# Optimization experiments

Measured on AMD Instinct MI355X. Metric: run time of the kernel, lower is better.

## Reference

```python
import jax, jax.numpy as jnp
import numpy as np

B, S, D, H = 4, 2048, 1024, 16
HD = D // H


def setup_inputs() -> dict:
    key = jax.random.key(0)
    ks = jax.random.split(key, 9)
    s = 1.0 / np.sqrt(D)
    return {
        "x": jax.random.normal(ks[0], (B, S, D), dtype=jnp.float32),
        "Wq": jax.random.uniform(ks[1], (D, D), jnp.float32, -s, s),
        "bq": jax.random.uniform(ks[2], (D,), jnp.float32, -s, s),
        "Wk": jax.random.uniform(ks[3], (D, D), jnp.float32, -s, s),
        "bk": jax.random.uniform(ks[4], (D,), jnp.float32, -s, s),
        "Wv": jax.random.uniform(ks[5], (D, D), jnp.float32, -s, s),
        "bv": jax.random.uniform(ks[6], (D,), jnp.float32, -s, s),
        "Wo": jax.random.uniform(ks[7], (D, D), jnp.float32, -s, s),
        "bo": jax.random.uniform(ks[8], (D,), jnp.float32, -s, s),
    }


def reference(x, Wq, bq, Wk, bk, Wv, bv, Wo, bo):
    b, s, _ = x.shape
    # projections (torch Linear: y = x @ W.T + b; here W stored as [D,D], use x@W for equivalent math)
    q = (x @ Wq + bq).reshape(b, s, H, HD).transpose(0, 2, 1, 3)  # [b,h,s,hd]
    k = (x @ Wk + bk).reshape(b, s, H, HD).transpose(0, 2, 1, 3)
    v = (x @ Wv + bv).reshape(b, s, H, HD).transpose(0, 2, 1, 3)
    scale = 1.0 / np.sqrt(HD).astype(np.float32)
    scores = jnp.einsum("bhqd,bhkd->bhqk", q, k) * scale  # [b,h,s,s]
    attn = jax.nn.softmax(scores, axis=-1)
    out = jnp.einsum("bhqk,bhkd->bhqd", attn, v)  # [b,h,s,hd]
    out = out.transpose(0, 2, 1, 3).reshape(b, s, D)
    return out @ Wo + bo
```

## Files before the change

kernel.cpp:

```cpp
#include <hip/hip_runtime.h>
#include <hip/hip_bf16.h>

#define NB 4
#define NS 2048
#define ND 1024
#define NH 16
#define NHD 64
#define NM (NB * NS)

typedef __attribute__((ext_vector_type(8))) short bf16x8;
typedef __attribute__((ext_vector_type(4))) float f32x4;
typedef __attribute__((ext_vector_type(16))) float f32x16;
typedef __attribute__((ext_vector_type(4))) unsigned int u32x4;

typedef const unsigned int __attribute__((address_space(1)))* gas_t;
typedef unsigned int __attribute__((address_space(3)))* las_t;

__device__ __forceinline__ void gload_lds16(const void* g, void* l) {
  __builtin_amdgcn_global_load_lds((gas_t)g, (las_t)l, 16, 0, 0);
}

__device__ __forceinline__ unsigned short f2bf(float f) {
  union { __hip_bfloat16 h; unsigned short u; } cv;
  cv.h = __float2bfloat16(f);
  return cv.u;
}

__device__ __forceinline__ unsigned int cvtpk(float a, float b) {
  unsigned int r;
  asm("v_cvt_pk_bf16_f32 %0, %1, %2" : "=v"(r) : "v"(a), "v"(b));
  return r;
}

__device__ __forceinline__ float fexp2(float x) {
  return __builtin_amdgcn_exp2f(x);
}

__global__ __launch_bounds__(256) void convert_x(
    const float* __restrict__ in, uint4* __restrict__ out) {
  const int c = blockIdx.x * 256 + threadIdx.x;
  const float4 a = *(const float4*)(in + (size_t)c * 8);
  const float4 b = *(const float4*)(in + (size_t)c * 8 + 4);
  uint4 u;
  u.x = cvtpk(a.x, a.y); u.y = cvtpk(a.z, a.w);
  u.z = cvtpk(b.x, b.y); u.w = cvtpk(b.z, b.w);
  out[c] = u;
}

__global__ __launch_bounds__(256) void transpose_qkv(
    const float* __restrict__ Wq, const float* __restrict__ Wk,
    const float* __restrict__ Wv, unsigned short* __restrict__ out) {
  __shared__ float tile[64][65];
  const int t = threadIdx.x;
  const int bx = blockIdx.x;
  const int by = blockIdx.y;
  const int which = by >> 4;
  const float* in = which == 0 ? Wq : (which == 1 ? Wk : Wv);
  const int byl = by & 15;
#pragma unroll
  for (int j = 0; j < 4; ++j) {
    const int lin = j * 1024 + t * 4;
    const int r = lin >> 6, c = lin & 63;
    float4 v = *(const float4*)(in + (size_t)(bx * 64 + r) * ND + byl * 64 + c);
    tile[r][c + 0] = v.x; tile[r][c + 1] = v.y;
    tile[r][c + 2] = v.z; tile[r][c + 3] = v.w;
  }
  __syncthreads();
#pragma unroll
  for (int j = 0; j < 4; ++j) {
    const int lin = j * 1024 + t * 4;
    const int r = lin >> 6, c = lin & 63;
    uint2 u;
    u.x = cvtpk(tile[c + 0][r], tile[c + 1][r]);
    u.y = cvtpk(tile[c + 2][r], tile[c + 3][r]);
    *(uint2*)(out + (size_t)(by * 64 + r) * ND + bx * 64 + c) = u;
  }
}

__global__ __launch_bounds__(256) void transpose_w(
    const float* __restrict__ in, unsigned short* __restrict__ out) {
  __shared__ float tile[64][65];
  const int t = threadIdx.x;
  const int bx = blockIdx.x, by = blockIdx.y;
#pragma unroll
  for (int j = 0; j < 4; ++j) {
    const int lin = j * 1024 + t * 4;
    const int r = lin >> 6, c = lin & 63;
    float4 v = *(const float4*)(in + (size_t)(bx * 64 + r) * ND + by * 64 + c);
    tile[r][c + 0] = v.x; tile[r][c + 1] = v.y;
    tile[r][c + 2] = v.z; tile[r][c + 3] = v.w;
  }
  __syncthreads();
#pragma unroll
  for (int j = 0; j < 4; ++j) {
    const int lin = j * 1024 + t * 4;
    const int r = lin >> 6, c = lin & 63;
    uint2 u;
    u.x = cvtpk(tile[c + 0][r], tile[c + 1][r]);
    u.y = cvtpk(tile[c + 2][r], tile[c + 3][r]);
    *(uint2*)(out + (size_t)(by * 64 + r) * ND + bx * 64 + c) = u;
  }
}

__global__ __launch_bounds__(256) void gemm_qkv(
    const unsigned short* __restrict__ Ab, const unsigned short* __restrict__ BT,
    const float* __restrict__ bq, const float* __restrict__ bk,
    const float* __restrict__ bv, unsigned short* __restrict__ Qb,
    unsigned short* __restrict__ Kb, unsigned short* __restrict__ VTb) {
  __shared__ unsigned short As[128 * 32];
  __shared__ unsigned short Bs[128 * 32];
  const int t = threadIdx.x;
  const int w = blockIdx.x;
  const int xcd = w & 7, idx = w >> 3;
  const int mblk = xcd + ((idx / 24) << 3);
  const int nblk = idx % 24;
  const int m0 = mblk * 128, n0 = nblk * 128;
  const int lane = t & 63, wid = t >> 6;
  const int wm = (wid >> 1) * 64, wn = (wid & 1) * 64;
  const int lr = lane & 15, lg = lane >> 4;

  const f32x4 zero4 = {0.f, 0.f, 0.f, 0.f};
  f32x4 acc[4][4];
#pragma unroll
  for (int i = 0; i < 4; ++i)
#pragma unroll
    for (int j = 0; j < 4; ++j) acc[i][j] = zero4;

  for (int k0 = 0; k0 < ND; k0 += 32) {
    __syncthreads();
#pragma unroll
    for (int j = 0; j < 2; ++j) {
      const int idx2 = j * 256 + t;
      const int row = idx2 >> 2, cs = idx2 & 3;
      const int cg = cs ^ ((row >> 1) & 3);
      gload_lds16(BT + (size_t)(n0 + row) * ND + k0 + cg * 8, &Bs[idx2 * 8]);
      gload_lds16(Ab + (size_t)(m0 + row) * ND + k0 + cg * 8, &As[idx2 * 8]);
    }
    __syncthreads();

    bf16x8 af[4], bv4[4];
#pragma unroll
    for (int mi = 0; mi < 4; ++mi) {
      const int row = wm + mi * 16 + lr;
      const int slot = lg ^ ((row >> 1) & 3);
      af[mi] = *(const bf16x8*)&As[row * 32 + slot * 8];
    }
#pragma unroll
    for (int ni = 0; ni < 4; ++ni) {
      const int row = wn + ni * 16 + lr;
      const int slot = lg ^ ((row >> 1) & 3);
      bv4[ni] = *(const bf16x8*)&Bs[row * 32 + slot * 8];
    }
    __builtin_amdgcn_s_setprio(1);
#pragma unroll
    for (int mi = 0; mi < 4; ++mi)
#pragma unroll
      for (int ni = 0; ni < 4; ++ni)
        acc[mi][ni] = __builtin_amdgcn_mfma_f32_16x16x32_bf16(
            af[mi], bv4[ni], acc[mi][ni], 0, 0, 0);
    __builtin_amdgcn_s_setprio(0);
  }

#pragma unroll
  for (int mi = 0; mi < 4; ++mi) {
#pragma unroll
    for (int ni = 0; ni < 4; ++ni) {
      const int mbase = m0 + wm + mi * 16 + lg * 4;
      const int n = n0 + wn + ni * 16 + lr;
      const int which = n >> 10, nl = n & 1023;
      const int h = nl >> 6, hd = nl & 63;
      const float bval = which == 0 ? bq[nl] : (which == 1 ? bk[nl] : bv[nl]);
      float vo[4];
#pragma unroll
      for (int i = 0; i < 4; ++i) {
        vo[i] = acc[mi][ni][i] + bval;
        if (which == 0) vo[i] *= 0.18033688f;
      }
      if (which < 2) {
        unsigned short* dst = which == 0 ? Qb : Kb;
#pragma unroll
        for (int i = 0; i < 4; ++i) {
          const int m = mbase + i;
          const int b = m >> 11, s = m & (NS - 1);
          dst[(((size_t)b * NH + h) * NS + s) * NHD + hd] = f2bf(vo[i]);
        }
      } else {
        const int b = mbase >> 11, s = mbase & (NS - 1);
        ushort4 o;
        o.x = f2bf(vo[0]); o.y = f2bf(vo[1]);
        o.z = f2bf(vo[2]); o.w = f2bf(vo[3]);
        *(ushort4*)&VTb[(((size_t)b * NH + h) * NHD + hd) * NS + s] = o;
      }
    }
  }
}

__global__ __launch_bounds__(256) void gemm_out(
    const unsigned short* __restrict__ Ab, const unsigned short* __restrict__ BT,
    const float* __restrict__ bias, float* __restrict__ Cf) {
  __shared__ unsigned short As[128 * 32];
  __shared__ unsigned short Bs[128 * 32];
  const int t = threadIdx.x;
  const int w = blockIdx.x;
  const int mblk = (w & 7) + ((w >> 6) << 3);
  const int nblk = (w >> 3) & 7;
  const int m0 = mblk * 128, n0 = nblk * 128;
  const int lane = t & 63, wid = t >> 6;
  const int wm = (wid >> 1) * 64, wn = (wid & 1) * 64;
  const int lr = lane & 15, lg = lane >> 4;

  const f32x4 zero4 = {0.f, 0.f, 0.f, 0.f};
  f32x4 acc[4][4];
#pragma unroll
  for (int i = 0; i < 4; ++i)
#pragma unroll
    for (int j = 0; j < 4; ++j) acc[i][j] = zero4;

  for (int k0 = 0; k0 < ND; k0 += 32) {
    __syncthreads();
#pragma unroll
    for (int j = 0; j < 2; ++j) {
      const int idx2 = j * 256 + t;
      const int row = idx2 >> 2, cs = idx2 & 3;
      const int cg = cs ^ ((row >> 1) & 3);
      gload_lds16(BT + (size_t)(n0 + row) * ND + k0 + cg * 8, &Bs[idx2 * 8]);
      gload_lds16(Ab + (size_t)(m0 + row) * ND + k0 + cg * 8, &As[idx2 * 8]);
    }
    __syncthreads();

    bf16x8 af[4], bv4[4];
#pragma unroll
    for (int mi = 0; mi < 4; ++mi) {
      const int row = wm + mi * 16 + lr;
      const int slot = lg ^ ((row >> 1) & 3);
      af[mi] = *(const bf16x8*)&As[row * 32 + slot * 8];
    }
#pragma unroll
    for (int ni = 0; ni < 4; ++ni) {
      const int row = wn + ni * 16 + lr;
      const int slot = lg ^ ((row >> 1) & 3);
      bv4[ni] = *(const bf16x8*)&Bs[row * 32 + slot * 8];
    }
    __builtin_amdgcn_s_setprio(1);
#pragma unroll
    for (int mi = 0; mi < 4; ++mi)
#pragma unroll
      for (int ni = 0; ni < 4; ++ni)
        acc[mi][ni] = __builtin_amdgcn_mfma_f32_16x16x32_bf16(
            af[mi], bv4[ni], acc[mi][ni], 0, 0, 0);
    __builtin_amdgcn_s_setprio(0);
  }

#pragma unroll
  for (int mi = 0; mi < 4; ++mi) {
#pragma unroll
    for (int ni = 0; ni < 4; ++ni) {
      const int mbase = m0 + wm + mi * 16 + lg * 4;
      const int n = n0 + wn + ni * 16 + lr;
      const float bval = bias[n];
#pragma unroll
      for (int i = 0; i < 4; ++i)
        Cf[(size_t)(mbase + i) * ND + n] = acc[mi][ni][i] + bval;
    }
  }
}

__global__ __launch_bounds__(512) void attn_mfma(
    const unsigned short* __restrict__ Qb, const unsigned short* __restrict__ Kb,
    const unsigned short* __restrict__ VTb, unsigned short* __restrict__ Aout) {
  __shared__ unsigned short S[32768];
  const int t = threadIdx.x, lane = t & 63, wid = t >> 6;
  const int lq = lane & 31, h = lane >> 5;
  const int w = blockIdx.x;
  const int xcd = w & 7, idx = w >> 3;
  const int bh = xcd + ((idx >> 3) << 3);
  const int qtile = idx & 7;
  const size_t hoff = (size_t)bh * NS * NHD;
  const int q0w = qtile * 256 + wid * 32;

  bf16x8 qf[4];
#pragma unroll
  for (int kc = 0; kc < 4; ++kc)
    qf[kc] = *(const bf16x8*)(Qb + hoff + (size_t)(q0w + lq) * NHD + kc * 16 + h * 8);

  const unsigned short* gK[2];
  const unsigned short* gV[2];
  unsigned short* lK[2];
  unsigned short* lV[2];
#pragma unroll
  for (int j = 0; j < 2; ++j) {
    const int c16 = wid * 2 + j;
    gK[j] = Kb + hoff + (size_t)((c16 & 3) * 32 + lq) * NHD + (c16 >> 2) * 16 + h * 8;
    lK[j] = &S[c16 * 512];
    gV[j] = VTb + hoff + (size_t)((c16 & 1) * 32 + lq) * NS + (c16 >> 1) * 16 + h * 8;
    lV[j] = &S[16384 + c16 * 512];
  }

  f32x16 z16 = 0.f;
  f32x16 oacc0 = 0.f, oacc1 = 0.f, lacc = 0.f;
  const short oneb = (short)0x3F80;
  const bf16x8 ones = {oneb, oneb, oneb, oneb, oneb, oneb, oneb, oneb};

  auto stage = [&](int bufofs, int tl) {
    const int kt = (2 * qtile + tl) & 15;
    const size_t kOff = (size_t)kt * (128 * NHD);
    const size_t vOff = (size_t)kt * 128;
#pragma unroll
    for (int j = 0; j < 2; ++j) {
      gload_lds16(gK[j] + kOff, lK[j] + bufofs);
      gload_lds16(gV[j] + vOff, lV[j] + bufofs);
    }
  };

  auto compute = [&](int bufofs) {
    const unsigned short* kb = &S[bufofs] + lane * 8;
    const unsigned short* vb = &S[16384 + bufofs] + lane * 8;
#pragma unroll
    for (int sb = 0; sb < 4; ++sb) {
      __builtin_amdgcn_s_setprio(1);
      f32x16 s;
      {
        bf16x8 k0 = *(const bf16x8*)(kb + sb * 512);
        s = __builtin_amdgcn_mfma_f32_32x32x16_bf16(k0, qf[0], z16, 0, 0, 0);
        bf16x8 k1 = *(const bf16x8*)(kb + sb * 512 + 2048);
        s = __builtin_amdgcn_mfma_f32_32x32x16_bf16(k1, qf[1], s, 0, 0, 0);
        bf16x8 k2 = *(const bf16x8*)(kb + sb * 512 + 4096);
        s = __builtin_amdgcn_mfma_f32_32x32x16_bf16(k2, qf[2], s, 0, 0, 0);
        bf16x8 k3 = *(const bf16x8*)(kb + sb * 512 + 6144);
        s = __builtin_amdgcn_mfma_f32_32x32x16_bf16(k3, qf[3], s, 0, 0, 0);
      }
      __builtin_amdgcn_s_setprio(0);

      unsigned int a0, a1, b0, b1, c0, c1, d0, d1;
      a0 = cvtpk(fexp2(s[0]), fexp2(s[1]));
      a1 = cvtpk(fexp2(s[2]), fexp2(s[3]));
      b0 = cvtpk(fexp2(s[4]), fexp2(s[5]));
      b1 = cvtpk(fexp2(s[6]), fexp2(s[7]));
      c0 = cvtpk(fexp2(s[8]), fexp2(s[9]));
      c1 = cvtpk(fexp2(s[10]), fexp2(s[11]));
      d0 = cvtpk(fexp2(s[12]), fexp2(s[13]));
      d1 = cvtpk(fexp2(s[14]), fexp2(s[15]));
      asm("v_permlane32_swap_b32 %0, %1" : "+v"(a0), "+v"(b0));
      asm("v_permlane32_swap_b32 %0, %1" : "+v"(a1), "+v"(b1));
      asm("v_permlane32_swap_b32 %0, %1" : "+v"(c0), "+v"(d0));
      asm("v_permlane32_swap_b32 %0, %1" : "+v"(c1), "+v"(d1));
      u32x4 plo_u = {a0, a1, b0, b1};
      u32x4 phi_u = {c0, c1, d0, d1};
      const bf16x8 plo = __builtin_bit_cast(bf16x8, plo_u);
      const bf16x8 phi = __builtin_bit_cast(bf16x8, phi_u);

      const int cA = sb * 2048;
      __builtin_amdgcn_s_setprio(1);
      {
        bf16x8 v0 = *(const bf16x8*)(vb + cA);
        oacc0 = __builtin_amdgcn_mfma_f32_32x32x16_bf16(v0, plo, oacc0, 0, 0, 0);
        bf16x8 v1 = *(const bf16x8*)(vb + cA + 512);
        oacc1 = __builtin_amdgcn_mfma_f32_32x32x16_bf16(v1, plo, oacc1, 0, 0, 0);
        lacc = __builtin_amdgcn_mfma_f32_32x32x16_bf16(ones, plo, lacc, 0, 0, 0);
        bf16x8 v2 = *(const bf16x8*)(vb + cA + 1024);
        oacc0 = __builtin_amdgcn_mfma_f32_32x32x16_bf16(v2, phi, oacc0, 0, 0, 0);
        bf16x8 v3 = *(const bf16x8*)(vb + cA + 1536);
        oacc1 = __builtin_amdgcn_mfma_f32_32x32x16_bf16(v3, phi, oacc1, 0, 0, 0);
        lacc = __builtin_amdgcn_mfma_f32_32x32x16_bf16(ones, phi, lacc, 0, 0, 0);
      }
      __builtin_amdgcn_s_setprio(0);
    }
  };

  stage(0, 0);
  __syncthreads();

  for (int i = 0; i < 8; ++i) {
    stage(8192, 2 * i + 1);
    compute(0);
    __syncthreads();
    if (i < 7) stage(0, 2 * i + 2);
    compute(8192);
    __syncthreads();
  }

  const float inv = 1.0f / lacc[0];
  unsigned short* Olds = &S[wid * 2304];
#pragma unroll
  for (int rr = 0; rr < 8; ++rr) {
    const int dl = 2 * (rr & 1) + 8 * (rr >> 1) + 4 * h;
    *(unsigned int*)&Olds[lq * 72 + dl] =
        cvtpk(oacc0[2 * rr] * inv, oacc0[2 * rr + 1] * inv);
    *(unsigned int*)&Olds[lq * 72 + 32 + dl] =
        cvtpk(oacc1[2 * rr] * inv, oacc1[2 * rr + 1] * inv);
  }
  const int b = bh >> 4, hh = bh & 15;
#pragma unroll
  for (int jj = 0; jj < 4; ++jj) {
    const int ci = jj * 64 + lane;
    const int q = ci >> 3, slot = ci & 7;
    const uint4 ov = *(const uint4*)&Olds[q * 72 + slot * 8];
    const int m = b * NS + q0w + q;
    *(uint4*)&Aout[(size_t)m * ND + hh * NHD + slot * 8] = ov;
  }
}

extern "C" void kernel_launch(void* const* d_in, const int* in_sizes, int n_in,
                              void* d_out, int out_size, void* d_ws,
                              size_t ws_size, hipStream_t stream) {
  const float* x  = (const float*)d_in[0];
  const float* Wq = (const float*)d_in[1];
  const float* bq = (const float*)d_in[2];
  const float* Wk = (const float*)d_in[3];
  const float* bk = (const float*)d_in[4];
  const float* Wv = (const float*)d_in[5];
  const float* bv = (const float*)d_in[6];
  const float* Wo = (const float*)d_in[7];
  const float* bo = (const float*)d_in[8];
  float* out = (float*)d_out;

  const size_t BIG = (size_t)NM * ND;
  unsigned short* Qb    = (unsigned short*)d_ws;
  unsigned short* Kb    = Qb + BIG;
  unsigned short* VTb   = Kb + BIG;
  unsigned short* Aattn = VTb + BIG;
  unsigned short* WTqkv = Aattn;
  unsigned short* WTo   = Qb;
  unsigned short* xb    = (unsigned short*)d_out;

  convert_x<<<4096, 256, 0, stream>>>(x, (uint4*)xb);
  transpose_qkv<<<dim3(16, 48), 256, 0, stream>>>(Wq, Wk, Wv, WTqkv);
  gemm_qkv<<<1536, 256, 0, stream>>>(xb, WTqkv, bq, bk, bv, Qb, Kb, VTb);

  attn_mfma<<<512, 512, 0, stream>>>(Qb, Kb, VTb, Aattn);

  transpose_w<<<dim3(16, 16), 256, 0, stream>>>(Wo, WTo);
  gemm_out<<<512, 256, 0, stream>>>(Aattn, WTo, bo, out);
}
```

Measured before the change: 190.2 us.

## Double-buffer LDS tiles in projection GEMMs and remap QKV block order

```diff
diff --git a/kernel.cpp b/kernel.cpp
--- a/kernel.cpp
+++ b/kernel.cpp
@@ -107,13 +107,13 @@
     const float* __restrict__ bq, const float* __restrict__ bk,
     const float* __restrict__ bv, unsigned short* __restrict__ Qb,
     unsigned short* __restrict__ Kb, unsigned short* __restrict__ VTb) {
-  __shared__ unsigned short As[128 * 32];
-  __shared__ unsigned short Bs[128 * 32];
+  __shared__ unsigned short As[2][128 * 32];
+  __shared__ unsigned short Bs[2][128 * 32];
   const int t = threadIdx.x;
   const int w = blockIdx.x;
   const int xcd = w & 7, idx = w >> 3;
-  const int mblk = xcd + ((idx / 24) << 3);
-  const int nblk = idx % 24;
+  const int nblk = xcd * 3 + idx % 3;
+  const int mblk = idx / 3;
   const int m0 = mblk * 128, n0 = nblk * 128;
   const int lane = t & 63, wid = t >> 6;
   const int wm = (wid >> 1) * 64, wn = (wid & 1) * 64;
@@ -126,30 +126,30 @@
 #pragma unroll
     for (int j = 0; j < 4; ++j) acc[i][j] = zero4;
 
-  for (int k0 = 0; k0 < ND; k0 += 32) {
-    __syncthreads();
+  auto stage = [&](int k0, int buf) {
 #pragma unroll
     for (int j = 0; j < 2; ++j) {
       const int idx2 = j * 256 + t;
       const int row = idx2 >> 2, cs = idx2 & 3;
       const int cg = cs ^ ((row >> 1) & 3);
-      gload_lds16(BT + (size_t)(n0 + row) * ND + k0 + cg * 8, &Bs[idx2 * 8]);
-      gload_lds16(Ab + (size_t)(m0 + row) * ND + k0 + cg * 8, &As[idx2 * 8]);
-    }
-    __syncthreads();
-
+      gload_lds16(BT + (size_t)(n0 + row) * ND + k0 + cg * 8, &Bs[buf][idx2 * 8]);
+      gload_lds16(Ab + (size_t)(m0 + row) * ND + k0 + cg * 8, &As[buf][idx2 * 8]);
+    }
+  };
+
+  auto compute = [&](int buf) {
     bf16x8 af[4], bv4[4];
 #pragma unroll
     for (int mi = 0; mi < 4; ++mi) {
       const int row = wm + mi * 16 + lr;
       const int slot = lg ^ ((row >> 1) & 3);
-      af[mi] = *(const bf16x8*)&As[row * 32 + slot * 8];
+      af[mi] = *(const bf16x8*)&As[buf][row * 32 + slot * 8];
     }
 #pragma unroll
     for (int ni = 0; ni < 4; ++ni) {
       const int row = wn + ni * 16 + lr;
       const int slot = lg ^ ((row >> 1) & 3);
-      bv4[ni] = *(const bf16x8*)&Bs[row * 32 + slot * 8];
+      bv4[ni] = *(const bf16x8*)&Bs[buf][row * 32 + slot * 8];
     }
     __builtin_amdgcn_s_setprio(1);
 #pragma unroll
@@ -159,6 +159,17 @@
         acc[mi][ni] = __builtin_amdgcn_mfma_f32_16x16x32_bf16(
             af[mi], bv4[ni], acc[mi][ni], 0, 0, 0);
     __builtin_amdgcn_s_setprio(0);
+  };
+
+  stage(0, 0);
+  __syncthreads();
+  for (int k0 = 0; k0 < ND; k0 += 64) {
+    stage(k0 + 32, 1);
+    compute(0);
+    __syncthreads();
+    if (k0 + 64 < ND) stage(k0 + 64, 0);
+    compute(1);
+    __syncthreads();
   }
 
 #pragma unroll
@@ -198,8 +209,8 @@
 __global__ __launch_bounds__(256) void gemm_out(
     const unsigned short* __restrict__ Ab, const unsigned short* __restrict__ BT,
     const float* __restrict__ bias, float* __restrict__ Cf) {
-  __shared__ unsigned short As[128 * 32];
-  __shared__ unsigned short Bs[128 * 32];
+  __shared__ unsigned short As[2][128 * 32];
+  __shared__ unsigned short Bs[2][128 * 32];
   const int t = threadIdx.x;
   const int w = blockIdx.x;
   const int mblk = (w & 7) + ((w >> 6) << 3);
@@ -216,30 +227,30 @@
 #pragma unroll
     for (int j = 0; j < 4; ++j) acc[i][j] = zero4;
 
-  for (int k0 = 0; k0 < ND; k0 += 32) {
-    __syncthreads();
+  auto stage = [&](int k0, int buf) {
 #pragma unroll
     for (int j = 0; j < 2; ++j) {
       const int idx2 = j * 256 + t;
       const int row = idx2 >> 2, cs = idx2 & 3;
       const int cg = cs ^ ((row >> 1) & 3);
-      gload_lds16(BT + (size_t)(n0 + row) * ND + k0 + cg * 8, &Bs[idx2 * 8]);
-      gload_lds16(Ab + (size_t)(m0 + row) * ND + k0 + cg * 8, &As[idx2 * 8]);
-    }
-    __syncthreads();
-
+      gload_lds16(BT + (size_t)(n0 + row) * ND + k0 + cg * 8, &Bs[buf][idx2 * 8]);
+      gload_lds16(Ab + (size_t)(m0 + row) * ND + k0 + cg * 8, &As[buf][idx2 * 8]);
+    }
+  };
+
+  auto compute = [&](int buf) {
     bf16x8 af[4], bv4[4];
 #pragma unroll
     for (int mi = 0; mi < 4; ++mi) {
       const int row = wm + mi * 16 + lr;
       const int slot = lg ^ ((row >> 1) & 3);
-      af[mi] = *(const bf16x8*)&As[row * 32 + slot * 8];
+      af[mi] = *(const bf16x8*)&As[buf][row * 32 + slot * 8];
     }
 #pragma unroll
     for (int ni = 0; ni < 4; ++ni) {
       const int row = wn + ni * 16 + lr;
       const int slot = lg ^ ((row >> 1) & 3);
-      bv4[ni] = *(const bf16x8*)&Bs[row * 32 + slot * 8];
+      bv4[ni] = *(const bf16x8*)&Bs[buf][row * 32 + slot * 8];
     }
     __builtin_amdgcn_s_setprio(1);
 #pragma unroll
@@ -249,6 +260,17 @@
         acc[mi][ni] = __builtin_amdgcn_mfma_f32_16x16x32_bf16(
             af[mi], bv4[ni], acc[mi][ni], 0, 0, 0);
     __builtin_amdgcn_s_setprio(0);
+  };
+
+  stage(0, 0);
+  __syncthreads();
+  for (int k0 = 0; k0 < ND; k0 += 64) {
+    stage(k0 + 32, 1);
+    compute(0);
+    __syncthreads();
+    if (k0 + 64 < ND) stage(k0 + 64, 0);
+    compute(1);
+    __syncthreads();
   }
 
 #pragma unroll
```

After: 190.8 us. No clear change (+0.3%).

## Give each attention wave two 32-query tiles and halve block threads

Applied to the files above, without the earlier changes.

```diff
diff --git a/kernel.cpp b/kernel.cpp
--- a/kernel.cpp
+++ b/kernel.cpp
@@ -265,7 +265,7 @@
   }
 }
 
-__global__ __launch_bounds__(512) void attn_mfma(
+__global__ __launch_bounds__(256) void attn_mfma(
     const unsigned short* __restrict__ Qb, const unsigned short* __restrict__ Kb,
     const unsigned short* __restrict__ VTb, unsigned short* __restrict__ Aout) {
   __shared__ unsigned short S[32768];
@@ -276,20 +276,22 @@
   const int bh = xcd + ((idx >> 3) << 3);
   const int qtile = idx & 7;
   const size_t hoff = (size_t)bh * NS * NHD;
-  const int q0w = qtile * 256 + wid * 32;
-
-  bf16x8 qf[4];
-#pragma unroll
-  for (int kc = 0; kc < 4; ++kc)
-    qf[kc] = *(const bf16x8*)(Qb + hoff + (size_t)(q0w + lq) * NHD + kc * 16 + h * 8);
-
-  const unsigned short* gK[2];
-  const unsigned short* gV[2];
-  unsigned short* lK[2];
-  unsigned short* lV[2];
-#pragma unroll
-  for (int j = 0; j < 2; ++j) {
-    const int c16 = wid * 2 + j;
+  const int q0w = qtile * 256 + wid * 64;
+
+  bf16x8 qfa[4], qfb[4];
+#pragma unroll
+  for (int kc = 0; kc < 4; ++kc) {
+    qfa[kc] = *(const bf16x8*)(Qb + hoff + (size_t)(q0w + lq) * NHD + kc * 16 + h * 8);
+    qfb[kc] = *(const bf16x8*)(Qb + hoff + (size_t)(q0w + 32 + lq) * NHD + kc * 16 + h * 8);
+  }
+
+  const unsigned short* gK[4];
+  const unsigned short* gV[4];
+  unsigned short* lK[4];
+  unsigned short* lV[4];
+#pragma unroll
+  for (int j = 0; j < 4; ++j) {
+    const int c16 = wid * 4 + j;
     gK[j] = Kb + hoff + (size_t)((c16 & 3) * 32 + lq) * NHD + (c16 >> 2) * 16 + h * 8;
     lK[j] = &S[c16 * 512];
     gV[j] = VTb + hoff + (size_t)((c16 & 1) * 32 + lq) * NS + (c16 >> 1) * 16 + h * 8;
@@ -297,7 +299,8 @@
   }
 
   f32x16 z16 = 0.f;
-  f32x16 oacc0 = 0.f, oacc1 = 0.f, lacc = 0.f;
+  f32x16 oA0 = 0.f, oA1 = 0.f, oB0 = 0.f, oB1 = 0.f;
+  f32x16 lA = 0.f, lB = 0.f;
   const short oneb = (short)0x3F80;
   const bf16x8 ones = {oneb, oneb, oneb, oneb, oneb, oneb, oneb, oneb};
 
@@ -306,7 +309,7 @@
     const size_t kOff = (size_t)kt * (128 * NHD);
     const size_t vOff = (size_t)kt * 128;
 #pragma unroll
-    for (int j = 0; j < 2; ++j) {
+    for (int j = 0; j < 4; ++j) {
       gload_lds16(gK[j] + kOff, lK[j] + bufofs);
       gload_lds16(gV[j] + vOff, lV[j] + bufofs);
     }
@@ -318,50 +321,78 @@
 #pragma unroll
     for (int sb = 0; sb < 4; ++sb) {
       __builtin_amdgcn_s_setprio(1);
-      f32x16 s;
+      f32x16 sA, sB;
       {
         bf16x8 k0 = *(const bf16x8*)(kb + sb * 512);
-        s = __builtin_amdgcn_mfma_f32_32x32x16_bf16(k0, qf[0], z16, 0, 0, 0);
+        sA = __builtin_amdgcn_mfma_f32_32x32x16_bf16(k0, qfa[0], z16, 0, 0, 0);
+        sB = __builtin_amdgcn_mfma_f32_32x32x16_bf16(k0, qfb[0], z16, 0, 0, 0);
         bf16x8 k1 = *(const bf16x8*)(kb + sb * 512 + 2048);
-        s = __builtin_amdgcn_mfma_f32_32x32x16_bf16(k1, qf[1], s, 0, 0, 0);
+        sA = __builtin_amdgcn_mfma_f32_32x32x16_bf16(k1, qfa[1], sA, 0, 0, 0);
+        sB = __builtin_amdgcn_mfma_f32_32x32x16_bf16(k1, qfb[1], sB, 0, 0, 0);
         bf16x8 k2 = *(const bf16x8*)(kb + sb * 512 + 4096);
-        s = __builtin_amdgcn_mfma_f32_32x32x16_bf16(k2, qf[2], s, 0, 0, 0);
+        sA = __builtin_amdgcn_mfma_f32_32x32x16_bf16(k2, qfa[2], sA, 0, 0, 0);
+        sB = __builtin_amdgcn_mfma_f32_32x32x16_bf16(k2, qfb[2], sB, 0, 0, 0);
         bf16x8 k3 = *(const bf16x8*)(kb + sb * 512 + 6144);
-        s = __builtin_amdgcn_mfma_f32_32x32x16_bf16(k3, qf[3], s, 0, 0, 0);
+        sA = __builtin_amdgcn_mfma_f32_32x32x16_bf16(k3, qfa[3], sA, 0, 0, 0);
+        sB = __builtin_amdgcn_mfma_f32_32x32x16_bf16(k3, qfb[3], sB, 0, 0, 0);
       }
       __builtin_amdgcn_s_setprio(0);
 
-      unsigned int a0, a1, b0, b1, c0, c1, d0, d1;
-      a0 = cvtpk(fexp2(s[0]), fexp2(s[1]));
-      a1 = cvtpk(fexp2(s[2]), fexp2(s[3]));
-      b0 = cvtpk(fexp2(s[4]), fexp2(s[5]));
-      b1 = cvtpk(fexp2(s[6]), fexp2(s[7]));
-      c0 = cvtpk(fexp2(s[8]), fexp2(s[9]));
-      c1 = cvtpk(fexp2(s[10]), fexp2(s[11]));
-      d0 = cvtpk(fexp2(s[12]), fexp2(s[13]));
-      d1 = cvtpk(fexp2(s[14]), fexp2(s[15]));
-      asm("v_permlane32_swap_b32 %0, %1" : "+v"(a0), "+v"(b0));
-      asm("v_permlane32_swap_b32 %0, %1" : "+v"(a1), "+v"(b1));
-      asm("v_permlane32_swap_b32 %0, %1" : "+v"(c0), "+v"(d0));
-      asm("v_permlane32_swap_b32 %0, %1" : "+v"(c1), "+v"(d1));
-      u32x4 plo_u = {a0, a1, b0, b1};
-      u32x4 phi_u = {c0, c1, d0, d1};
-      const bf16x8 plo = __builtin_bit_cast(bf16x8, plo_u);
-      const bf16x8 phi = __builtin_bit_cast(bf16x8, phi_u);
+      unsigned int aA0, aA1, bA0, bA1, cA0, cA1, dA0, dA1;
+      aA0 = cvtpk(fexp2(sA[0]), fexp2(sA[1]));
+      aA1 = cvtpk(fexp2(sA[2]), fexp2(sA[3]));
+      bA0 = cvtpk(fexp2(sA[4]), fexp2(sA[5]));
+      bA1 = cvtpk(fexp2(sA[6]), fexp2(sA[7]));
+      cA0 = cvtpk(fexp2(sA[8]), fexp2(sA[9]));
+      cA1 = cvtpk(fexp2(sA[10]), fexp2(sA[11]));
+      dA0 = cvtpk(fexp2(sA[12]), fexp2(sA[13]));
+      dA1 = cvtpk(fexp2(sA[14]), fexp2(sA[15]));
+      asm("v_permlane32_swap_b32 %0, %1" : "+v"(aA0), "+v"(bA0));
+      asm("v_permlane32_swap_b32 %0, %1" : "+v"(aA1), "+v"(bA1));
+      asm("v_permlane32_swap_b32 %0, %1" : "+v"(cA0), "+v"(dA0));
+      asm("v_permlane32_swap_b32 %0, %1" : "+v"(cA1), "+v"(dA1));
+      u32x4 ploAu = {aA0, aA1, bA0, bA1};
+      u32x4 phiAu = {cA0, cA1, dA0, dA1};
+      const bf16x8 ploA = __builtin_bit_cast(bf16x8, ploAu);
+      const bf16x8 phiA = __builtin_bit_cast(bf16x8, phiAu);
+
+      unsigned int aB0, aB1, bB0, bB1, cB0, cB1, dB0, dB1;
+      aB0 = cvtpk(fexp2(sB[0]), fexp2(sB[1]));
+      aB1 = cvtpk(fexp2(sB[2]), fexp2(sB[3]));
+      bB0 = cvtpk(fexp2(sB[4]), fexp2(sB[5]));
+      bB1 = cvtpk(fexp2(sB[6]), fexp2(sB[7]));
+      cB0 = cvtpk(fexp2(sB[8]), fexp2(sB[9]));
+      cB1 = cvtpk(fexp2(sB[10]), fexp2(sB[11]));
+      dB0 = cvtpk(fexp2(sB[12]), fexp2(sB[13]));
+      dB1 = cvtpk(fexp2(sB[14]), fexp2(sB[15]));
+      asm("v_permlane32_swap_b32 %0, %1" : "+v"(aB0), "+v"(bB0));
+      asm("v_permlane32_swap_b32 %0, %1" : "+v"(aB1), "+v"(bB1));
+      asm("v_permlane32_swap_b32 %0, %1" : "+v"(cB0), "+v"(dB0));
+      asm("v_permlane32_swap_b32 %0, %1" : "+v"(cB1), "+v"(dB1));
+      u32x4 ploBu = {aB0, aB1, bB0, bB1};
+      u32x4 phiBu = {cB0, cB1, dB0, dB1};
+      const bf16x8 ploB = __builtin_bit_cast(bf16x8, ploBu);
+      const bf16x8 phiB = __builtin_bit_cast(bf16x8, phiBu);
 
       const int cA = sb * 2048;
       __builtin_amdgcn_s_setprio(1);
       {
         bf16x8 v0 = *(const bf16x8*)(vb + cA);
-        oacc0 = __builtin_amdgcn_mfma_f32_32x32x16_bf16(v0, plo, oacc0, 0, 0, 0);
+        oA0 = __builtin_amdgcn_mfma_f32_32x32x16_bf16(v0, ploA, oA0, 0, 0, 0);
+        oB0 = __builtin_amdgcn_mfma_f32_32x32x16_bf16(v0, ploB, oB0, 0, 0, 0);
         bf16x8 v1 = *(const bf16x8*)(vb + cA + 512);
-        oacc1 = __builtin_amdgcn_mfma_f32_32x32x16_bf16(v1, plo, oacc1, 0, 0, 0);
-        lacc = __builtin_amdgcn_mfma_f32_32x32x16_bf16(ones, plo, lacc, 0, 0, 0);
+        oA1 = __builtin_amdgcn_mfma_f32_32x32x16_bf16(v1, ploA, oA1, 0, 0, 0);
+        oB1 = __builtin_amdgcn_mfma_f32_32x32x16_bf16(v1, ploB, oB1, 0, 0, 0);
+        lA = __builtin_amdgcn_mfma_f32_32x32x16_bf16(ones, ploA, lA, 0, 0, 0);
+        lB = __builtin_amdgcn_mfma_f32_32x32x16_bf16(ones, ploB, lB, 0, 0, 0);
         bf16x8 v2 = *(const bf16x8*)(vb + cA + 1024);
-        oacc0 = __builtin_amdgcn_mfma_f32_32x32x16_bf16(v2, phi, oacc0, 0, 0, 0);
+        oA0 = __builtin_amdgcn_mfma_f32_32x32x16_bf16(v2, phiA, oA0, 0, 0, 0);
+        oB0 = __builtin_amdgcn_mfma_f32_32x32x16_bf16(v2, phiB, oB0, 0, 0, 0);
         bf16x8 v3 = *(const bf16x8*)(vb + cA + 1536);
-        oacc1 = __builtin_amdgcn_mfma_f32_32x32x16_bf16(v3, phi, oacc1, 0, 0, 0);
-        lacc = __builtin_amdgcn_mfma_f32_32x32x16_bf16(ones, phi, lacc, 0, 0, 0);
+        oA1 = __builtin_amdgcn_mfma_f32_32x32x16_bf16(v3, phiA, oA1, 0, 0, 0);
+        oB1 = __builtin_amdgcn_mfma_f32_32x32x16_bf16(v3, phiB, oB1, 0, 0, 0);
+        lA = __builtin_amdgcn_mfma_f32_32x32x16_bf16(ones, phiA, lA, 0, 0, 0);
+        lB = __builtin_amdgcn_mfma_f32_32x32x16_bf16(ones, phiB, lB, 0, 0, 0);
       }
       __builtin_amdgcn_s_setprio(0);
     }
@@ -379,19 +410,24 @@
     __syncthreads();
   }
 
-  const float inv = 1.0f / lacc[0];
-  unsigned short* Olds = &S[wid * 2304];
+  const float invA = 1.0f / lA[0];
+  const float invB = 1.0f / lB[0];
+  unsigned short* Olds = &S[wid * 4608];
 #pragma unroll
   for (int rr = 0; rr < 8; ++rr) {
     const int dl = 2 * (rr & 1) + 8 * (rr >> 1) + 4 * h;
     *(unsigned int*)&Olds[lq * 72 + dl] =
-        cvtpk(oacc0[2 * rr] * inv, oacc0[2 * rr + 1] * inv);
+        cvtpk(oA0[2 * rr] * invA, oA0[2 * rr + 1] * invA);
     *(unsigned int*)&Olds[lq * 72 + 32 + dl] =
-        cvtpk(oacc1[2 * rr] * inv, oacc1[2 * rr + 1] * inv);
+        cvtpk(oA1[2 * rr] * invA, oA1[2 * rr + 1] * invA);
+    *(unsigned int*)&Olds[(32 + lq) * 72 + dl] =
+        cvtpk(oB0[2 * rr] * invB, oB0[2 * rr + 1] * invB);
+    *(unsigned int*)&Olds[(32 + lq) * 72 + 32 + dl] =
+        cvtpk(oB1[2 * rr] * invB, oB1[2 * rr + 1] * invB);
   }
   const int b = bh >> 4, hh = bh & 15;
 #pragma unroll
-  for (int jj = 0; jj < 4; ++jj) {
+  for (int jj = 0; jj < 8; ++jj) {
     const int ci = jj * 64 + lane;
     const int q = ci >> 3, slot = ci & 7;
     const uint4 ov = *(const uint4*)&Olds[q * 72 + slot * 8];
@@ -427,7 +463,7 @@
   transpose_qkv<<<dim3(16, 48), 256, 0, stream>>>(Wq, Wk, Wv, WTqkv);
   gemm_qkv<<<1536, 256, 0, stream>>>(xb, WTqkv, bq, bk, bv, Qb, Kb, VTb);
 
-  attn_mfma<<<512, 512, 0, stream>>>(Qb, Kb, VTb, Aattn);
+  attn_mfma<<<512, 256, 0, stream>>>(Qb, Kb, VTb, Aattn);
 
   transpose_w<<<dim3(16, 16), 256, 0, stream>>>(Wo, WTo);
   gemm_out<<<512, 256, 0, stream>>>(Aattn, WTo, bo, out);
```

New measurement: 218.0 us. +14.6%, slower.
